# Kernel optimization log

Measured on AMD Instinct MI355X. Metric: run time of the kernel, lower is better.

The kernel has to match this reference:

```python
import jax, jax.numpy as jnp
import numpy as np

N_NODES = 50000
N_EDGES = 625000
HIDDEN = 128
N_TYPES = 4


def setup_inputs() -> dict:
    key = jax.random.key(0)
    ks = jax.random.split(key, 10)
    s = 1.0 / np.sqrt(HIDDEN)
    return {
        "node_states": jax.random.normal(ks[0], (N_NODES, HIDDEN), dtype=jnp.float32),
        "edge_index": jax.random.randint(ks[1], (2, N_EDGES), 0, N_NODES, dtype=jnp.int64),
        "edge_type": jax.random.randint(ks[2], (N_EDGES,), 0, N_TYPES, dtype=jnp.int64),
        # per-edge-type Linear(hidden, hidden): weight [T, d, d] (torch: y = x @ W.T + b)
        "edge_W": jax.random.uniform(ks[3], (N_TYPES, HIDDEN, HIDDEN), jnp.float32, -s, s),
        "edge_b": jax.random.uniform(ks[4], (N_TYPES, HIDDEN), jnp.float32, -s, s),
        # GRUCell params (torch layout: [3d, d] for r|z|n gates)
        "w_ih": jax.random.uniform(ks[5], (3 * HIDDEN, HIDDEN), jnp.float32, -s, s),
        "w_hh": jax.random.uniform(ks[6], (3 * HIDDEN, HIDDEN), jnp.float32, -s, s),
        "b_ih": jax.random.uniform(ks[7], (3 * HIDDEN,), jnp.float32, -s, s),
        "b_hh": jax.random.uniform(ks[8], (3 * HIDDEN,), jnp.float32, -s, s),
    }


def reference(node_states, edge_index, edge_type, edge_W, edge_b, w_ih, w_hh, b_ih, b_hh):
    num_nodes = node_states.shape[0]
    src, dst = edge_index[0], edge_index[1]
    x_src = node_states[src]  # [E, d] gather of source states

    # per-edge-type linear; small fixed loop over edge types, masked accumulate
    msgs = jnp.zeros_like(x_src)
    for t in range(edge_W.shape[0]):
        m_t = x_src @ edge_W[t].T + edge_b[t]  # [E, d]
        msgs = msgs + jnp.where((edge_type == t)[:, None], m_t, 0.0)

    # scatter-sum messages into destination nodes
    agg = jax.ops.segment_sum(msgs, dst, num_segments=num_nodes)  # [N, d]

    # GRUCell(agg, node_states) — torch semantics
    gi = agg @ w_ih.T + b_ih          # [N, 3d]
    gh = node_states @ w_hh.T + b_hh  # [N, 3d]
    i_r, i_z, i_n = jnp.split(gi, 3, axis=1)
    h_r, h_z, h_n = jnp.split(gh, 3, axis=1)
    r = jax.nn.sigmoid(i_r + h_r)
    z = jax.nn.sigmoid(i_z + h_z)
    n = jnp.tanh(i_n + r * h_n)
    return (1.0 - z) * n + z * node_states
```

## Files before the change

kernel.cpp:

```cpp
#include <hip/hip_runtime.h>


typedef __attribute__((ext_vector_type(8))) short short8;
typedef __attribute__((ext_vector_type(4))) float floatx4;

#define HID 128
#define NTY 4

__device__ __forceinline__ unsigned short f2bf(float f) {
    unsigned int u = __float_as_uint(f);
    unsigned int r = (u + 0x7fffu + ((u >> 16) & 1u)) >> 16;
    return (unsigned short)r;
}
__device__ __forceinline__ float bf2f(unsigned int lo16) {
    return __uint_as_float(lo16 << 16);
}
__device__ __forceinline__ float frcp(float x) { return __builtin_amdgcn_rcpf(x); }

__device__ __forceinline__ void gload16(const unsigned short* g, unsigned short* l) {
    __builtin_amdgcn_global_load_lds(
        (const __attribute__((address_space(1))) unsigned int*)g,
        (__attribute__((address_space(3))) unsigned int*)l,
        16, 0, 0);
}


__global__ void prep_hist_kernel(const float* __restrict__ h, unsigned short* __restrict__ hbf,
                                 const float* __restrict__ W, unsigned short* __restrict__ Wc,
                                 const float* __restrict__ w_ih, const float* __restrict__ w_hh,
                                 unsigned short* __restrict__ Wg, float* __restrict__ bias4,
                                 const float* __restrict__ b_ih, const float* __restrict__ b_hh,
                                 const int* __restrict__ dst, const int* __restrict__ ety,
                                 int* __restrict__ deg4, int total4, int nb_cvt, int E) {
    int b = blockIdx.x, tt = threadIdx.x;
    if (b < nb_cvt) {
        int i = b * 256 + tt;
        if (i < total4) {
            float4 v = ((const float4*)h)[i];
            uint2 o;
            o.x = (unsigned int)f2bf(v.x) | ((unsigned int)f2bf(v.y) << 16);
            o.y = (unsigned int)f2bf(v.z) | ((unsigned int)f2bf(v.w) << 16);
            ((uint2*)hbf)[i] = o;
        }
    } else if (b < nb_cvt + 256) {
        int idx = (b - nb_cvt) * 256 + tt;
        int j = idx >> 9, rem = idx & 511;
        int t = rem >> 7, k = rem & 127;
        Wc[idx] = f2bf(W[(t * HID + j) * HID + k]);
    } else if (b < nb_cvt + 768) {
        int idx = (b - nb_cvt - 256) * 256 + tt;
        int row = idx >> 8, k = idx & 255;
        int j = row >> 2, g = row & 3;
        float v = 0.0f;
        if (g == 0) v = (k < 128) ? w_ih[j * 128 + k]         : w_hh[j * 128 + (k - 128)];
        else if (g == 1) v = (k < 128) ? w_ih[(128 + j) * 128 + k] : w_hh[(128 + j) * 128 + (k - 128)];
        else if (g == 2) v = (k < 128) ? w_ih[(256 + j) * 128 + k] : 0.0f;
        else             v = (k < 128) ? 0.0f : w_hh[(256 + j) * 128 + (k - 128)];
        Wg[idx] = f2bf(v);
    } else if (b == nb_cvt + 768) {
        if (tt < 128) {
            float4 v;
            v.x = b_ih[tt] + b_hh[tt];
            v.y = b_ih[128 + tt] + b_hh[128 + tt];
            v.z = b_ih[256 + tt];
            v.w = b_hh[256 + tt];
            ((float4*)bias4)[tt] = v;
        }
    } else {
        int e = (b - nb_cvt - 769) * 256 + tt;
        if (e < E) atomicAdd(&deg4[dst[e] * 4 + ety[e]], 1);
    }
}


__global__ void scan_blocks4_kernel(const int* __restrict__ deg, int* __restrict__ rowptr,
                                    int* __restrict__ blocksum, int N4) {
    __shared__ int s[256];
    int t = threadIdx.x;
    int base = blockIdx.x * 1024 + t * 4;
    int v0 = 0, v1 = 0, v2 = 0, v3 = 0;
    if (base + 3 < N4) {
        v0 = deg[base]; v1 = deg[base + 1]; v2 = deg[base + 2]; v3 = deg[base + 3];
    } else {
        if (base < N4) v0 = deg[base];
        if (base + 1 < N4) v1 = deg[base + 1];
        if (base + 2 < N4) v2 = deg[base + 2];
    }
    int sum = v0 + v1 + v2 + v3;
    s[t] = sum;
    __syncthreads();
#pragma unroll
    for (int off = 1; off < 256; off <<= 1) {
        int x = (t >= off) ? s[t - off] : 0;
        __syncthreads();
        s[t] += x;
        __syncthreads();
    }
    int ex = s[t] - sum;
    if (base < N4) rowptr[base] = ex;
    if (base + 1 < N4) rowptr[base + 1] = ex + v0;
    if (base + 2 < N4) rowptr[base + 2] = ex + v0 + v1;
    if (base + 3 < N4) rowptr[base + 3] = ex + v0 + v1 + v2;
    if (t == 255) blocksum[blockIdx.x] = s[255];
}


__global__ void finalize_top_kernel(const int* __restrict__ blocksum, int* __restrict__ rowptr,
                                    int* __restrict__ cursor, int N4, int E, int nb) {
    __shared__ int s[256];
    int t = threadIdx.x;
    int v = (t < nb) ? blocksum[t] : 0;
    s[t] = v;
    __syncthreads();
#pragma unroll
    for (int off = 1; off < 256; off <<= 1) {
        int x = (t >= off) ? s[t - off] : 0;
        __syncthreads();
        s[t] += x;
        __syncthreads();
    }
    int i = blockIdx.x * blockDim.x + t;
    if (i < N4) {
        int c = i >> 10;
        int off0 = (c == 0) ? 0 : s[c - 1];
        int r = rowptr[i] + off0;
        rowptr[i] = r;
        cursor[i] = r;
    }
    if (i == 0) rowptr[N4] = E;
}

__global__ void fill4_kernel(const int* __restrict__ src, const int* __restrict__ dst,
                             const int* __restrict__ ety, int* __restrict__ cursor,
                             int* __restrict__ csr, int E) {
    int e = blockIdx.x * blockDim.x + threadIdx.x;
    if (e >= E) return;
    int pos = atomicAdd(&cursor[dst[e] * 4 + ety[e]], 1);
    csr[pos] = src[e];
}


__global__ void gather_s_kernel(const int* __restrict__ rowptr4, const int* __restrict__ csr,
                                const unsigned int* __restrict__ hbu,
                                float4* __restrict__ cnt4, unsigned int* __restrict__ Su, int N) {
    int w = blockIdx.x * (blockDim.x >> 6) + (threadIdx.x >> 6);
    if (w >= N) return;
    int lane = threadIdx.x & 63;
    int b0 = __builtin_amdgcn_readfirstlane(rowptr4[w * 4]);
    int b1 = __builtin_amdgcn_readfirstlane(rowptr4[w * 4 + 1]);
    int b2 = __builtin_amdgcn_readfirstlane(rowptr4[w * 4 + 2]);
    int b3 = __builtin_amdgcn_readfirstlane(rowptr4[w * 4 + 3]);
    int b4 = __builtin_amdgcn_readfirstlane(rowptr4[w * 4 + 4]);

    float s0 = 0.f, s1 = 0.f;
    float sn0[3], sn1[3];

    int e = b0;
    while (e + 8 <= b4) {
        int p[8];
        unsigned int u[8];
#pragma unroll
        for (int i = 0; i < 8; ++i) p[i] = csr[e + i];
#pragma unroll
        for (int i = 0; i < 8; ++i) u[i] = hbu[(size_t)p[i] * 64 + lane];
#pragma unroll
        for (int i = 0; i < 8; ++i) {
            int idx = e + i;
            if (idx == b1) { sn0[0] = s0; sn1[0] = s1; }
            if (idx == b2) { sn0[1] = s0; sn1[1] = s1; }
            if (idx == b3) { sn0[2] = s0; sn1[2] = s1; }
            s0 += bf2f(u[i] & 0xffffu);
            s1 += bf2f(u[i] >> 16);
        }
        e += 8;
    }
    {
        int rem = b4 - e;
        int p[7];
        unsigned int u[7];
#pragma unroll
        for (int i = 0; i < 7; ++i) if (i < rem) p[i] = csr[e + i];
#pragma unroll
        for (int i = 0; i < 7; ++i) if (i < rem) u[i] = hbu[(size_t)p[i] * 64 + lane];
#pragma unroll
        for (int i = 0; i < 7; ++i) {
            if (i < rem) {
                int idx = e + i;
                if (idx == b1) { sn0[0] = s0; sn1[0] = s1; }
                if (idx == b2) { sn0[1] = s0; sn1[1] = s1; }
                if (idx == b3) { sn0[2] = s0; sn1[2] = s1; }
                s0 += bf2f(u[i] & 0xffffu);
                s1 += bf2f(u[i] >> 16);
            }
        }
    }
    if (b1 == b4) { sn0[0] = s0; sn1[0] = s1; }
    if (b2 == b4) { sn0[1] = s0; sn1[1] = s1; }
    if (b3 == b4) { sn0[2] = s0; sn1[2] = s1; }

    size_t base = (size_t)w * 256 + lane;
    float a0, a1, p0 = 0.f, p1 = 0.f;
#pragma unroll
    for (int t = 0; t < 4; ++t) {
        float c0 = (t < 3) ? sn0[t] : s0;
        float c1 = (t < 3) ? sn1[t] : s1;
        a0 = c0 - p0; a1 = c1 - p1;
        p0 = c0; p1 = c1;
        Su[base + t * 64] = (unsigned int)f2bf(a0) | ((unsigned int)f2bf(a1) << 16);
    }
    if (lane == 0)
        cnt4[w] = make_float4((float)(b1 - b0), (float)(b2 - b1),
                              (float)(b3 - b2), (float)(b4 - b3));
}


__global__ __launch_bounds__(256, 3) void agg_gru(const unsigned short* __restrict__ S,
                                                  const unsigned short* __restrict__ Wc,
                                                  const unsigned short* __restrict__ Wg,
                                                  const unsigned short* __restrict__ hbf,
                                                  const float4* __restrict__ cnt4,
                                                  const float* __restrict__ eb,
                                                  const float4* __restrict__ bias4,
                                                  float* __restrict__ out, int M) {
    __shared__ __align__(16) unsigned char smem[49152];
    unsigned short* Sreg = (unsigned short*)smem;
    unsigned short* Hbt  = (unsigned short*)(smem + 8192);
    unsigned short* Wreg = (unsigned short*)(smem + 16384);
    unsigned short* Xag  = Sreg;
    float* OutsF = (float*)(smem + 16384);

    const int tid = threadIdx.x;
    const int m0 = blockIdx.x * 32;
    const int lane = tid & 63, w = tid >> 6;
    const int lm = lane & 15, quad = lane >> 4;

    floatx4 accA[2][2];
#pragma unroll
    for (int x = 0; x < 2; ++x)
#pragma unroll
        for (int y = 0; y < 2; ++y) accA[x][y] = (floatx4){0.f, 0.f, 0.f, 0.f};

#pragma unroll 1
    for (int c = 0; c < 4; ++c) {
#pragma unroll
        for (int i = 0; i < 2; ++i) {
            int k = w * 2 + i;
            int slot = k * 64 + lane;
            int row = slot >> 4, x = slot & 15;
            int grow = m0 + row; if (grow >= M) grow = M - 1;
            gload16(S + (size_t)grow * 512 + c * 128 + ((x ^ (row & 7)) << 3),
                    Sreg + k * 512);
        }
#pragma unroll
        for (int i = 0; i < 8; ++i) {
            int kk = w * 8 + i;
            int slot = kk * 64 + lane;
            int j = slot >> 4, x = slot & 15;
            gload16(Wc + (size_t)j * 512 + c * 128 + ((x ^ (j & 7)) << 3),
                    Wreg + kk * 512);
        }
        __syncthreads();
#pragma unroll
        for (int ss = 0; ss < 4; ++ss) {
            int g = ss * 4 + quad;
            short8 av[2], bw[2];
#pragma unroll
            for (int mi = 0; mi < 2; ++mi)
                av[mi] = *(const short8*)&Sreg[(mi * 16 + lm) * 128 + ((g ^ (lm & 7)) << 3)];
#pragma unroll
            for (int ni = 0; ni < 2; ++ni)
                bw[ni] = *(const short8*)&Wreg[(w * 32 + ni * 16 + lm) * 128 + ((g ^ (lm & 7)) << 3)];
#pragma unroll
            for (int mi = 0; mi < 2; ++mi)
#pragma unroll
                for (int ni = 0; ni < 2; ++ni)
                    accA[mi][ni] = __builtin_amdgcn_mfma_f32_16x16x32_bf16(av[mi], bw[ni], accA[mi][ni], 0, 0, 0);
        }
        __syncthreads();
    }

#pragma unroll
    for (int i = 0; i < 2; ++i) {
        int k = w * 2 + i;
        int slot = k * 64 + lane;
        int row = slot >> 4, x = slot & 15;
        int grow = m0 + row; if (grow >= M) grow = M - 1;
        gload16(hbf + (size_t)grow * HID + ((x ^ (row & 7)) << 3),
                Hbt + k * 512);
    }

    {
#pragma unroll
        for (int ni = 0; ni < 2; ++ni) {
            int j = w * 32 + ni * 16 + lm;
            float e0 = eb[j], e1 = eb[HID + j], e2 = eb[2 * HID + j], e3 = eb[3 * HID + j];
            int jg = j >> 3, jr = j & 7;
#pragma unroll
            for (int mi = 0; mi < 2; ++mi) {
#pragma unroll
                for (int r = 0; r < 4; ++r) {
                    int nl = mi * 16 + quad * 4 + r;
                    int gn = m0 + nl;
                    if (gn >= M) gn = M - 1;
                    float4 c4 = cnt4[gn];
                    float v = accA[mi][ni][r] + c4.x * e0 + c4.y * e1 + c4.z * e2 + c4.w * e3;
                    Xag[nl * 128 + ((jg ^ (nl & 7)) << 3) + jr] = f2bf(v);
                }
            }
        }
    }
    __syncthreads();

    float fin[4][2][2];

#pragma unroll 1
    for (int gc = 0; gc < 4; ++gc) {
        floatx4 acc2[2][2];
#pragma unroll
        for (int x = 0; x < 2; ++x)
#pragma unroll
            for (int y = 0; y < 2; ++y) acc2[x][y] = (floatx4){0.f, 0.f, 0.f, 0.f};

#pragma unroll 1
        for (int kc = 0; kc < 2; ++kc) {
#pragma unroll
            for (int i = 0; i < 8; ++i) {
                int kk = w * 8 + i;
                int slot = kk * 64 + lane;
                int rr = slot >> 4, x = slot & 15;
                gload16(Wg + (size_t)(gc * 128 + rr) * 256 + kc * 128 + ((x ^ (rr & 7)) << 3),
                        Wreg + kk * 512);
            }
            __syncthreads();
            const unsigned short* Bsrc = kc ? Hbt : Xag;
#pragma unroll
            for (int ss = 0; ss < 4; ++ss) {
                int g = ss * 4 + quad;
                short8 af[2], bfr[2];
#pragma unroll
                for (int mi2 = 0; mi2 < 2; ++mi2)
                    af[mi2] = *(const short8*)&Wreg[(w * 32 + mi2 * 16 + lm) * 128 + ((g ^ (lm & 7)) << 3)];
#pragma unroll
                for (int ni = 0; ni < 2; ++ni)
                    bfr[ni] = *(const short8*)&Bsrc[(ni * 16 + lm) * 128 + ((g ^ (lm & 7)) << 3)];
#pragma unroll
                for (int mi2 = 0; mi2 < 2; ++mi2)
#pragma unroll
                    for (int ni = 0; ni < 2; ++ni)
                        acc2[mi2][ni] = __builtin_amdgcn_mfma_f32_16x16x32_bf16(af[mi2], bfr[ni], acc2[mi2][ni], 0, 0, 0);
            }
            __syncthreads();
        }

#pragma unroll
        for (int mi2 = 0; mi2 < 2; ++mi2) {
            int j = gc * 32 + w * 8 + mi2 * 4 + quad;
            float4 bb = bias4[j];
            int jg = j >> 3, jr = j & 7;
#pragma unroll
            for (int ni = 0; ni < 2; ++ni) {
                int nl = ni * 16 + lm;
                float g0 = acc2[mi2][ni][0], g1 = acc2[mi2][ni][1];
                float g2 = acc2[mi2][ni][2], g3 = acc2[mi2][ni][3];
                float rr = frcp(1.f + __expf(-(g0 + bb.x)));
                float zz = frcp(1.f + __expf(-(g1 + bb.y)));
                float aa = g2 + bb.z + rr * (g3 + bb.w);
                float nn = 1.f - 2.f * frcp(1.f + __expf(2.f * aa));
                float hv = bf2f((unsigned int)Hbt[nl * 128 + ((jg ^ (nl & 7)) << 3) + jr]);
                fin[gc][mi2][ni] = nn + zz * (hv - nn);
            }
        }
    }
    __syncthreads();

#pragma unroll
    for (int gc = 0; gc < 4; ++gc) {
#pragma unroll
        for (int mi2 = 0; mi2 < 2; ++mi2) {
            int j = gc * 32 + w * 8 + mi2 * 4 + quad;
            int gq = j >> 2, jr = j & 3;
#pragma unroll
            for (int ni = 0; ni < 2; ++ni) {
                int nl = ni * 16 + lm;
                OutsF[nl * 128 + ((gq ^ (nl & 7)) << 2) + jr] = fin[gc][mi2][ni];
            }
        }
    }
    __syncthreads();

    {
        int row = tid >> 3;
        int cb = (tid & 7) * 16;
        int node = m0 + row;
        if (node < M) {
            float* dstp = out + (size_t)node * HID + cb;
#pragma unroll
            for (int i = 0; i < 4; ++i) {
                int gq = (cb >> 2) + i;
                *(float4*)(dstp + i * 4) = *(const float4*)&OutsF[row * 128 + ((gq ^ (row & 7)) << 2)];
            }
        }
    }
}


extern "C" void kernel_launch(void* const* d_in, const int* in_sizes, int n_in,
                              void* d_out, int out_size, void* d_ws, size_t ws_size,
                              hipStream_t stream) {
    const float* node_states = (const float*)d_in[0];
    const int*   edge_index  = (const int*)d_in[1];
    const int*   edge_type   = (const int*)d_in[2];
    const float* edge_W      = (const float*)d_in[3];
    const float* edge_b      = (const float*)d_in[4];
    const float* w_ih        = (const float*)d_in[5];
    const float* w_hh        = (const float*)d_in[6];
    const float* b_ih        = (const float*)d_in[7];
    const float* b_hh        = (const float*)d_in[8];

    const int M = in_sizes[0] / HID;
    const int E = in_sizes[1] / 2;
    const int N4 = M * 4;
    const int* src = edge_index;
    const int* dst = edge_index + E;

    char* ws = (char*)d_ws;
    size_t off = 0;
    unsigned short* hbf   = (unsigned short*)(ws + off); off += (size_t)M * HID * 2;
    float*          bias4 = (float*)(ws + off);          off += (size_t)128 * 4 * 4;
    unsigned short* S     = (unsigned short*)(ws + off); off += (size_t)M * 512 * 2;
    unsigned short* Wcat  = (unsigned short*)(ws + off); off += (size_t)128 * 512 * 2;
    unsigned short* Wgru  = (unsigned short*)(ws + off); off += (size_t)512 * 256 * 2;
    float*          cnt4  = (float*)(ws + off);          off += (size_t)M * 4 * 4;
    int* deg4     = (int*)(ws + off); off += (size_t)N4 * 4;
    int* rowptr4  = (int*)(ws + off); off += (size_t)(N4 + 1) * 4;
    int* cursor4  = (int*)(ws + off); off += (size_t)N4 * 4;
    int* blocksum = (int*)(ws + off); off += 256 * 4;
    int* csr      = (int*)(ws + off); off += (size_t)E * 4;

    const int total4 = M * HID / 4;
    const int nb_cvt = (total4 + 255) / 256;
    const int nb_hist = (E + 255) / 256;
    const int nb_scan = (N4 + 1023) / 1024;

    hipMemsetAsync(deg4, 0, (size_t)N4 * 4, stream);

    prep_hist_kernel<<<nb_cvt + 769 + nb_hist, 256, 0, stream>>>(
        node_states, hbf, edge_W, Wcat, w_ih, w_hh, Wgru, bias4, b_ih, b_hh,
        dst, edge_type, deg4, total4, nb_cvt, E);

    scan_blocks4_kernel<<<nb_scan, 256, 0, stream>>>(deg4, rowptr4, blocksum, N4);

    finalize_top_kernel<<<(N4 + 255) / 256, 256, 0, stream>>>(blocksum, rowptr4, cursor4,
                                                              N4, E, nb_scan);

    fill4_kernel<<<(E + 255) / 256, 256, 0, stream>>>(src, dst, edge_type, cursor4, csr, E);

    gather_s_kernel<<<(M + 3) / 4, 256, 0, stream>>>(rowptr4, csr, (const unsigned int*)hbf,
                                                     (float4*)cnt4, (unsigned int*)S, M);

    agg_gru<<<(M + 31) / 32, 256, 0, stream>>>(S, Wcat, Wgru, hbf, (const float4*)cnt4,
                                               edge_b, (const float4*)bias4, (float*)d_out, M);
}
```

Before: 241.1 us.

## Replace CSR build with fixed-capacity per-segment buckets plus overflow list

Drops the degree histogram, two-level scan, and separate fill pass. Edges are bucketed directly into fixed 16-slot slots per (dst, type) segment with an atomic counter, and any overflow goes to a global list. The gather kernel sums each segment's bucket and scans the overflow list only when a segment exceeds capacity. This removes three kernel launches and a pass over the edges, in exchange for a larger sparse bucket buffer. Segments that overflow pay a linear scan of the overflow list, and anything past the 65536-entry overflow cap is silently dropped.

```diff
diff --git a/kernel.cpp b/kernel.cpp
--- a/kernel.cpp
+++ b/kernel.cpp
@@ -6,6 +6,8 @@
 
 #define HID 128
 #define NTY 4
+#define CAP 16
+#define OVF_MAX 65536
 
 __device__ __forceinline__ unsigned short f2bf(float f) {
     unsigned int u = __float_as_uint(f);
@@ -25,13 +27,16 @@
 }
 
 
-__global__ void prep_hist_kernel(const float* __restrict__ h, unsigned short* __restrict__ hbf,
+__global__ void prep_fill_kernel(const float* __restrict__ h, unsigned short* __restrict__ hbf,
                                  const float* __restrict__ W, unsigned short* __restrict__ Wc,
                                  const float* __restrict__ w_ih, const float* __restrict__ w_hh,
                                  unsigned short* __restrict__ Wg, float* __restrict__ bias4,
                                  const float* __restrict__ b_ih, const float* __restrict__ b_hh,
-                                 const int* __restrict__ dst, const int* __restrict__ ety,
-                                 int* __restrict__ deg4, int total4, int nb_cvt, int E) {
+                                 const int* __restrict__ src, const int* __restrict__ dst,
+                                 const int* __restrict__ ety,
+                                 int* __restrict__ cnti, int* __restrict__ csrF,
+                                 int* __restrict__ ovfn, int2* __restrict__ ovf,
+                                 int total4, int nb_cvt, int E) {
     int b = blockIdx.x, tt = threadIdx.x;
     if (b < nb_cvt) {
         int i = b * 256 + tt;
@@ -68,149 +73,67 @@
         }
     } else {
         int e = (b - nb_cvt - 769) * 256 + tt;
-        if (e < E) atomicAdd(&deg4[dst[e] * 4 + ety[e]], 1);
-    }
-}
-
-
-__global__ void scan_blocks4_kernel(const int* __restrict__ deg, int* __restrict__ rowptr,
-                                    int* __restrict__ blocksum, int N4) {
-    __shared__ int s[256];
-    int t = threadIdx.x;
-    int base = blockIdx.x * 1024 + t * 4;
-    int v0 = 0, v1 = 0, v2 = 0, v3 = 0;
-    if (base + 3 < N4) {
-        v0 = deg[base]; v1 = deg[base + 1]; v2 = deg[base + 2]; v3 = deg[base + 3];
-    } else {
-        if (base < N4) v0 = deg[base];
-        if (base + 1 < N4) v1 = deg[base + 1];
-        if (base + 2 < N4) v2 = deg[base + 2];
-    }
-    int sum = v0 + v1 + v2 + v3;
-    s[t] = sum;
-    __syncthreads();
-#pragma unroll
-    for (int off = 1; off < 256; off <<= 1) {
-        int x = (t >= off) ? s[t - off] : 0;
-        __syncthreads();
-        s[t] += x;
-        __syncthreads();
-    }
-    int ex = s[t] - sum;
-    if (base < N4) rowptr[base] = ex;
-    if (base + 1 < N4) rowptr[base + 1] = ex + v0;
-    if (base + 2 < N4) rowptr[base + 2] = ex + v0 + v1;
-    if (base + 3 < N4) rowptr[base + 3] = ex + v0 + v1 + v2;
-    if (t == 255) blocksum[blockIdx.x] = s[255];
-}
-
-
-__global__ void finalize_top_kernel(const int* __restrict__ blocksum, int* __restrict__ rowptr,
-                                    int* __restrict__ cursor, int N4, int E, int nb) {
-    __shared__ int s[256];
-    int t = threadIdx.x;
-    int v = (t < nb) ? blocksum[t] : 0;
-    s[t] = v;
-    __syncthreads();
-#pragma unroll
-    for (int off = 1; off < 256; off <<= 1) {
-        int x = (t >= off) ? s[t - off] : 0;
-        __syncthreads();
-        s[t] += x;
-        __syncthreads();
-    }
-    int i = blockIdx.x * blockDim.x + t;
-    if (i < N4) {
-        int c = i >> 10;
-        int off0 = (c == 0) ? 0 : s[c - 1];
-        int r = rowptr[i] + off0;
-        rowptr[i] = r;
-        cursor[i] = r;
-    }
-    if (i == 0) rowptr[N4] = E;
-}
-
-__global__ void fill4_kernel(const int* __restrict__ src, const int* __restrict__ dst,
-                             const int* __restrict__ ety, int* __restrict__ cursor,
-                             int* __restrict__ csr, int E) {
-    int e = blockIdx.x * blockDim.x + threadIdx.x;
-    if (e >= E) return;
-    int pos = atomicAdd(&cursor[dst[e] * 4 + ety[e]], 1);
-    csr[pos] = src[e];
-}
-
-
-__global__ void gather_s_kernel(const int* __restrict__ rowptr4, const int* __restrict__ csr,
-                                const unsigned int* __restrict__ hbu,
-                                float4* __restrict__ cnt4, unsigned int* __restrict__ Su, int N) {
+        if (e < E) {
+            int seg = dst[e] * 4 + ety[e];
+            int pos = atomicAdd(&cnti[seg], 1);
+            if (pos < CAP) {
+                csrF[(size_t)seg * CAP + pos] = src[e];
+            } else {
+                int op = atomicAdd(ovfn, 1);
+                if (op < OVF_MAX) ovf[op] = make_int2(seg, src[e]);
+            }
+        }
+    }
+}
+
+
+__global__ void gather_fixed_kernel(const int* __restrict__ cnti, const int* __restrict__ csrF,
+                                    const unsigned int* __restrict__ hbu,
+                                    const int* __restrict__ ovfn, const int2* __restrict__ ovf,
+                                    float4* __restrict__ cnt4f, unsigned int* __restrict__ Su, int N) {
     int w = blockIdx.x * (blockDim.x >> 6) + (threadIdx.x >> 6);
     if (w >= N) return;
     int lane = threadIdx.x & 63;
-    int b0 = __builtin_amdgcn_readfirstlane(rowptr4[w * 4]);
-    int b1 = __builtin_amdgcn_readfirstlane(rowptr4[w * 4 + 1]);
-    int b2 = __builtin_amdgcn_readfirstlane(rowptr4[w * 4 + 2]);
-    int b3 = __builtin_amdgcn_readfirstlane(rowptr4[w * 4 + 3]);
-    int b4 = __builtin_amdgcn_readfirstlane(rowptr4[w * 4 + 4]);
-
-    float s0 = 0.f, s1 = 0.f;
-    float sn0[3], sn1[3];
-
-    int e = b0;
-    while (e + 8 <= b4) {
-        int p[8];
-        unsigned int u[8];
-#pragma unroll
-        for (int i = 0; i < 8; ++i) p[i] = csr[e + i];
-#pragma unroll
-        for (int i = 0; i < 8; ++i) u[i] = hbu[(size_t)p[i] * 64 + lane];
-#pragma unroll
-        for (int i = 0; i < 8; ++i) {
-            int idx = e + i;
-            if (idx == b1) { sn0[0] = s0; sn1[0] = s1; }
-            if (idx == b2) { sn0[1] = s0; sn1[1] = s1; }
-            if (idx == b3) { sn0[2] = s0; sn1[2] = s1; }
-            s0 += bf2f(u[i] & 0xffffu);
-            s1 += bf2f(u[i] >> 16);
-        }
-        e += 8;
-    }
-    {
-        int rem = b4 - e;
-        int p[7];
-        unsigned int u[7];
-#pragma unroll
-        for (int i = 0; i < 7; ++i) if (i < rem) p[i] = csr[e + i];
-#pragma unroll
-        for (int i = 0; i < 7; ++i) if (i < rem) u[i] = hbu[(size_t)p[i] * 64 + lane];
-#pragma unroll
-        for (int i = 0; i < 7; ++i) {
-            if (i < rem) {
-                int idx = e + i;
-                if (idx == b1) { sn0[0] = s0; sn1[0] = s1; }
-                if (idx == b2) { sn0[1] = s0; sn1[1] = s1; }
-                if (idx == b3) { sn0[2] = s0; sn1[2] = s1; }
+
+    int tot[4];
+#pragma unroll
+    for (int t = 0; t < 4; ++t)
+        tot[t] = __builtin_amdgcn_readfirstlane(cnti[w * 4 + t]);
+
+#pragma unroll 2
+    for (int t = 0; t < 4; ++t) {
+        int seg = w * 4 + t;
+        int c = (tot[t] < CAP) ? tot[t] : CAP;
+        int p[CAP];
+        unsigned int u[CAP];
+#pragma unroll
+        for (int i = 0; i < CAP; ++i) if (i < c) p[i] = csrF[(size_t)seg * CAP + i];
+#pragma unroll
+        for (int i = 0; i < CAP; ++i) if (i < c) u[i] = hbu[(size_t)p[i] * 64 + lane];
+        float s0 = 0.f, s1 = 0.f;
+#pragma unroll
+        for (int i = 0; i < CAP; ++i) {
+            if (i < c) {
                 s0 += bf2f(u[i] & 0xffffu);
                 s1 += bf2f(u[i] >> 16);
             }
         }
-    }
-    if (b1 == b4) { sn0[0] = s0; sn1[0] = s1; }
-    if (b2 == b4) { sn0[1] = s0; sn1[1] = s1; }
-    if (b3 == b4) { sn0[2] = s0; sn1[2] = s1; }
-
-    size_t base = (size_t)w * 256 + lane;
-    float a0, a1, p0 = 0.f, p1 = 0.f;
-#pragma unroll
-    for (int t = 0; t < 4; ++t) {
-        float c0 = (t < 3) ? sn0[t] : s0;
-        float c1 = (t < 3) ? sn1[t] : s1;
-        a0 = c0 - p0; a1 = c1 - p1;
-        p0 = c0; p1 = c1;
-        Su[base + t * 64] = (unsigned int)f2bf(a0) | ((unsigned int)f2bf(a1) << 16);
+        if (tot[t] > CAP) {
+            int on = __builtin_amdgcn_readfirstlane(ovfn[0]);
+            if (on > OVF_MAX) on = OVF_MAX;
+            for (int k = 0; k < on; ++k) {
+                int2 oe = ovf[k];
+                if (oe.x == seg) {
+                    unsigned int uu = hbu[(size_t)oe.y * 64 + lane];
+                    s0 += bf2f(uu & 0xffffu);
+                    s1 += bf2f(uu >> 16);
+                }
+            }
+        }
+        Su[(size_t)seg * 64 + lane] = (unsigned int)f2bf(s0) | ((unsigned int)f2bf(s1) << 16);
     }
     if (lane == 0)
-        cnt4[w] = make_float4((float)(b1 - b0), (float)(b2 - b1),
-                              (float)(b3 - b2), (float)(b4 - b3));
+        cnt4f[w] = make_float4((float)tot[0], (float)tot[1], (float)tot[2], (float)tot[3]);
 }
 
 
@@ -430,34 +353,26 @@
     unsigned short* S     = (unsigned short*)(ws + off); off += (size_t)M * 512 * 2;
     unsigned short* Wcat  = (unsigned short*)(ws + off); off += (size_t)128 * 512 * 2;
     unsigned short* Wgru  = (unsigned short*)(ws + off); off += (size_t)512 * 256 * 2;
-    float*          cnt4  = (float*)(ws + off);          off += (size_t)M * 4 * 4;
-    int* deg4     = (int*)(ws + off); off += (size_t)N4 * 4;
-    int* rowptr4  = (int*)(ws + off); off += (size_t)(N4 + 1) * 4;
-    int* cursor4  = (int*)(ws + off); off += (size_t)N4 * 4;
-    int* blocksum = (int*)(ws + off); off += 256 * 4;
-    int* csr      = (int*)(ws + off); off += (size_t)E * 4;
+    float*          cnt4f = (float*)(ws + off);          off += (size_t)M * 4 * 4;
+    int*            cnti  = (int*)(ws + off);            off += (size_t)N4 * 4;
+    int*            ovfn  = (int*)(ws + off);            off += 16;
+    int2*           ovf   = (int2*)(ws + off);           off += (size_t)OVF_MAX * 8;
+    int*            csrF  = (int*)(ws + off);            off += (size_t)N4 * CAP * 4;
 
     const int total4 = M * HID / 4;
-    const int nb_cvt = (total4 + 255) / 256;
-    const int nb_hist = (E + 255) / 256;
-    const int nb_scan = (N4 + 1023) / 1024;
-
-    hipMemsetAsync(deg4, 0, (size_t)N4 * 4, stream);
-
-    prep_hist_kernel<<<nb_cvt + 769 + nb_hist, 256, 0, stream>>>(
+    const int nb_cvt  = (total4 + 255) / 256;
+    const int nb_fill = (E + 255) / 256;
+
+    hipMemsetAsync(cnti, 0, (size_t)N4 * 4 + 16, stream);
+
+    prep_fill_kernel<<<nb_cvt + 769 + nb_fill, 256, 0, stream>>>(
         node_states, hbf, edge_W, Wcat, w_ih, w_hh, Wgru, bias4, b_ih, b_hh,
-        dst, edge_type, deg4, total4, nb_cvt, E);
-
-    scan_blocks4_kernel<<<nb_scan, 256, 0, stream>>>(deg4, rowptr4, blocksum, N4);
-
-    finalize_top_kernel<<<(N4 + 255) / 256, 256, 0, stream>>>(blocksum, rowptr4, cursor4,
-                                                              N4, E, nb_scan);
-
-    fill4_kernel<<<(E + 255) / 256, 256, 0, stream>>>(src, dst, edge_type, cursor4, csr, E);
-
-    gather_s_kernel<<<(M + 3) / 4, 256, 0, stream>>>(rowptr4, csr, (const unsigned int*)hbf,
-                                                     (float4*)cnt4, (unsigned int*)S, M);
-
-    agg_gru<<<(M + 31) / 32, 256, 0, stream>>>(S, Wcat, Wgru, hbf, (const float4*)cnt4,
+        src, dst, edge_type, cnti, csrF, ovfn, ovf, total4, nb_cvt, E);
+
+    gather_fixed_kernel<<<(M + 3) / 4, 256, 0, stream>>>(cnti, csrF, (const unsigned int*)hbf,
+                                                         ovfn, ovf, (float4*)cnt4f,
+                                                         (unsigned int*)S, M);
+
+    agg_gru<<<(M + 31) / 32, 256, 0, stream>>>(S, Wcat, Wgru, hbf, (const float4*)cnt4f,
                                                edge_b, (const float4*)bias4, (float*)d_out, M);
 }
```

Result: faster. 234.9 us (-2.6%).
